# Kernel optimization log

Hardware: AMD Instinct MI355X
Metric: run time of the kernel (lower is better)

Reference implementation:

```python
import jax, jax.numpy as jnp
import numpy as np

B, H, W, CIN, COUT, KH, KW = 8, 256, 256, 64, 64, 3, 3

def setup_inputs() -> dict:
    key = jax.random.key(0)
    k1, k2 = jax.random.split(key)
    inputs = jax.random.normal(k1, (B, H, W, CIN), dtype=jnp.float32)
    kernel = jax.random.normal(k2, (CIN, COUT, KH, KW), dtype=jnp.float32)
    return {"inputs": inputs, "kernel": kernel}

def reference(inputs, kernel):
    # Stride-1 transposed convolution with 'full' output size:
    # out[b, p, q, co] = sum_{ci,i,j} inputs[b, i, j, ci] * kernel[ci, co, p-i, q-j]
    # which is a full (mathematical) convolution. lax performs cross-correlation,
    # so flip the kernel spatially and pad by (k-1) on each side.
    kh, kw = kernel.shape[2], kernel.shape[3]
    k_flipped = jnp.flip(kernel, axis=(2, 3))
    out = jax.lax.conv_general_dilated(
        inputs, k_flipped,
        window_strides=(1, 1),
        padding=[(kh - 1, kh - 1), (kw - 1, kw - 1)],
        dimension_numbers=("NHWC", "IOHW", "NHWC"))
    # out: [B, H+KH-1, W+KW-1, COUT]; original call() adds no bias.
    return out
```

## Files before the change

### kernel.cpp

```cpp
#include <hip/hip_runtime.h>
#include <hip/hip_bf16.h>


#define OH 258
#define OW 258

typedef __bf16 bf16x8 __attribute__((ext_vector_type(8)));
typedef float  f32x4  __attribute__((ext_vector_type(4)));

__global__ void prep_w_kernel(const float* __restrict__ k, __bf16* __restrict__ wsW) {
    int i = blockIdx.x * 256 + threadIdx.x;
    int c  = i & 31;
    int co = (i >> 5) & 63;
    int st = i >> 11;
    int s   = st & 1;
    int tap = st >> 1;
    int kh = tap / 3, kw = tap % 3;
    float v = k[(s * 32 + c) * 576 + co * 9 + kh * 3 + kw];
    wsW[i] = (__bf16)v;
}

__global__ __launch_bounds__(512, 4)
void tconv_kernel(const float* __restrict__ in, const __bf16* __restrict__ wsW,
                  float* __restrict__ out) {
    __shared__ __bf16 lds_in[612 * 64];

    const int tid = threadIdx.x;
    const int b  = blockIdx.z;
    const int p0 = blockIdx.y * 32;
    const int q0 = blockIdx.x * 16;

    #pragma unroll 1
    for (int it = tid; it < 612 * 8; it += 512) {
        int pix = it >> 3, c8 = it & 7;
        int r = pix / 18, c = pix - r * 18;
        int ip = p0 - 2 + r, iq = q0 - 2 + c;
        f32x4 v0 = {0.f,0.f,0.f,0.f}, v1 = {0.f,0.f,0.f,0.f};
        if ((unsigned)ip < 256u && (unsigned)iq < 256u) {
            const float* g = in + (((size_t)b * 256 + ip) * 256 + iq) * 64 + c8 * 8;
            v0 = *(const f32x4*)g;
            v1 = *(const f32x4*)(g + 4);
        }
        bf16x8 w;
        w[0]=(__bf16)v0[0]; w[1]=(__bf16)v0[1]; w[2]=(__bf16)v0[2]; w[3]=(__bf16)v0[3];
        w[4]=(__bf16)v1[0]; w[5]=(__bf16)v1[1]; w[6]=(__bf16)v1[2]; w[7]=(__bf16)v1[3];
        *(bf16x8*)&lds_in[pix * 64 + (c8 ^ (pix & 7)) * 8] = w;
    }
    __syncthreads();

    const int wv = tid >> 6, lane = tid & 63;
    const int ml = lane & 15, h = lane >> 4;
    const int woff = ml * 32 + h * 8;

    f32x4 acc[4][4] = {};

    #pragma unroll 1
    for (int tap = 0; tap < 9; ++tap) {
        const int kh = tap / 3, kw = tap - kh * 3;
        const __bf16* wt = wsW + tap * 4096;
        #pragma unroll
        for (int s = 0; s < 2; ++s) {
            bf16x8 bfr[4];
            #pragma unroll
            for (int nt = 0; nt < 4; ++nt)
                bfr[nt] = *(const bf16x8*)(wt + s * 2048 + nt * 512 + woff);
            const int j = s * 4 + h;
            #pragma unroll
            for (int mt = 0; mt < 4; ++mt) {
                int row = wv * 4 + mt + 2 - kh;
                int pix = row * 18 + (2 - kw) + ml;
                bf16x8 afr = *(const bf16x8*)&lds_in[pix * 64 + ((j ^ (pix & 7)) * 8)];
                #pragma unroll
                for (int nt = 0; nt < 4; ++nt)
                    acc[mt][nt] = __builtin_amdgcn_mfma_f32_16x16x32_bf16(
                        afr, bfr[nt], acc[mt][nt], 0, 0, 0);
            }
        }
    }

    #pragma unroll
    for (int mt = 0; mt < 4; ++mt) {
        int p = p0 + wv * 4 + mt;
        if (p < OH) {
            int qb = q0 + h * 4;
            #pragma unroll
            for (int nt = 0; nt < 4; ++nt) {
                float* op = out + (((size_t)b * OH + p) * OW + qb) * 64 + nt * 16 + ml;
                #pragma unroll
                for (int r = 0; r < 4; ++r)
                    if (qb + r < OW) op[(size_t)r * 64] = acc[mt][nt][r];
            }
        }
    }
}

extern "C" void kernel_launch(void* const* d_in, const int* in_sizes, int n_in,
                              void* d_out, int out_size, void* d_ws, size_t ws_size,
                              hipStream_t stream) {
    (void)in_sizes; (void)n_in; (void)out_size; (void)ws_size;
    const float* in   = (const float*)d_in[0];
    const float* kern = (const float*)d_in[1];
    float* out = (float*)d_out;
    __bf16* wsW = (__bf16*)d_ws;

    prep_w_kernel<<<144, 256, 0, stream>>>(kern, wsW);
    dim3 grid(17, 9, 8);
    tconv_kernel<<<grid, 512, 0, stream>>>(in, wsW, out);
}
```

Measured before the change: 277.7 us.

## Halve output tile height and batch global loads for more occupancy

Each block now covers 16 output rows instead of 32, which halves the LDS input tile (324 pixels instead of 612) and the per-wave accumulators. The grid grows to 17x17x8 and launch bounds ask for 6 blocks per CU. The staging loop is unrolled in groups of three so several global loads are in flight before the bf16 conversion and LDS stores. The cost is more halo recomputation per output row (18/16 instead of 34/32), more blocks, and fewer MFMAs per B-fragment load.

```diff
diff --git a/kernel.cpp b/kernel.cpp
--- a/kernel.cpp
+++ b/kernel.cpp
@@ -20,39 +20,57 @@
     wsW[i] = (__bf16)v;
 }
 
-__global__ __launch_bounds__(512, 4)
+__global__ __launch_bounds__(512, 6)
 void tconv_kernel(const float* __restrict__ in, const __bf16* __restrict__ wsW,
                   float* __restrict__ out) {
-    __shared__ __bf16 lds_in[612 * 64];
+    __shared__ __bf16 lds_in[324 * 64];
 
     const int tid = threadIdx.x;
     const int b  = blockIdx.z;
-    const int p0 = blockIdx.y * 32;
+    const int p0 = blockIdx.y * 16;
     const int q0 = blockIdx.x * 16;
 
     #pragma unroll 1
-    for (int it = tid; it < 612 * 8; it += 512) {
-        int pix = it >> 3, c8 = it & 7;
-        int r = pix / 18, c = pix - r * 18;
-        int ip = p0 - 2 + r, iq = q0 - 2 + c;
-        f32x4 v0 = {0.f,0.f,0.f,0.f}, v1 = {0.f,0.f,0.f,0.f};
-        if ((unsigned)ip < 256u && (unsigned)iq < 256u) {
-            const float* g = in + (((size_t)b * 256 + ip) * 256 + iq) * 64 + c8 * 8;
-            v0 = *(const f32x4*)g;
-            v1 = *(const f32x4*)(g + 4);
+    for (int kk = 0; kk < 6; kk += 3) {
+        f32x4 v0[3], v1[3];
+        int soff[3];
+        #pragma unroll
+        for (int u = 0; u < 3; ++u) {
+            const int k = kk + u;
+            const int it = tid + k * 512;
+            const bool act = (k < 5) || (tid < 32);
+            int pix = it >> 3, c8 = it & 7;
+            int r = pix / 18, c = pix - r * 18;
+            int ip = p0 - 2 + r, iq = q0 - 2 + c;
+            f32x4 z = {0.f, 0.f, 0.f, 0.f};
+            v0[u] = z; v1[u] = z;
+            if (act && (unsigned)ip < 256u && (unsigned)iq < 256u) {
+                const float* g = in + (((size_t)b * 256 + ip) * 256 + iq) * 64 + c8 * 8;
+                v0[u] = *(const f32x4*)g;
+                v1[u] = *(const f32x4*)(g + 4);
+            }
+            soff[u] = pix * 64 + ((c8 ^ (pix & 7)) * 8);
         }
-        bf16x8 w;
-        w[0]=(__bf16)v0[0]; w[1]=(__bf16)v0[1]; w[2]=(__bf16)v0[2]; w[3]=(__bf16)v0[3];
-        w[4]=(__bf16)v1[0]; w[5]=(__bf16)v1[1]; w[6]=(__bf16)v1[2]; w[7]=(__bf16)v1[3];
-        *(bf16x8*)&lds_in[pix * 64 + (c8 ^ (pix & 7)) * 8] = w;
+        #pragma unroll
+        for (int u = 0; u < 3; ++u) {
+            const int k = kk + u;
+            const bool act = (k < 5) || (tid < 32);
+            if (act) {
+                bf16x8 w;
+                w[0]=(__bf16)v0[u][0]; w[1]=(__bf16)v0[u][1]; w[2]=(__bf16)v0[u][2]; w[3]=(__bf16)v0[u][3];
+                w[4]=(__bf16)v1[u][0]; w[5]=(__bf16)v1[u][1]; w[6]=(__bf16)v1[u][2]; w[7]=(__bf16)v1[u][3];
+                *(bf16x8*)&lds_in[soff[u]] = w;
+            }
+        }
     }
     __syncthreads();
 
     const int wv = tid >> 6, lane = tid & 63;
     const int ml = lane & 15, h = lane >> 4;
     const int woff = ml * 32 + h * 8;
+    const int rbase = wv * 2;
 
-    f32x4 acc[4][4] = {};
+    f32x4 acc[2][4] = {};
 
     #pragma unroll 1
     for (int tap = 0; tap < 9; ++tap) {
@@ -66,8 +84,8 @@
                 bfr[nt] = *(const bf16x8*)(wt + s * 2048 + nt * 512 + woff);
             const int j = s * 4 + h;
             #pragma unroll
-            for (int mt = 0; mt < 4; ++mt) {
-                int row = wv * 4 + mt + 2 - kh;
+            for (int mt = 0; mt < 2; ++mt) {
+                int row = rbase + mt + 2 - kh;
                 int pix = row * 18 + (2 - kw) + ml;
                 bf16x8 afr = *(const bf16x8*)&lds_in[pix * 64 + ((j ^ (pix & 7)) * 8)];
                 #pragma unroll
@@ -79,8 +97,8 @@
     }
 
     #pragma unroll
-    for (int mt = 0; mt < 4; ++mt) {
-        int p = p0 + wv * 4 + mt;
+    for (int mt = 0; mt < 2; ++mt) {
+        int p = p0 + rbase + mt;
         if (p < OH) {
             int qb = q0 + h * 4;
             #pragma unroll
@@ -104,6 +122,6 @@
     __bf16* wsW = (__bf16*)d_ws;
 
     prep_w_kernel<<<144, 256, 0, stream>>>(kern, wsW);
-    dim3 grid(17, 9, 8);
+    dim3 grid(17, 17, 8);
     tconv_kernel<<<grid, 512, 0, stream>>>(in, wsW, out);
 }
```

Result: slower. 292.7 us (+5.4%).

## Drop LDS staging; load input fragments directly from global into registers

Applied to the files above, without the earlier changes.

Removes the shared-memory input tile and the block barrier. Each wave now loads its A fragments straight from global memory per kw and channel half, converts them to bf16 in registers, and reuses six rows across the three kh taps. Blocks shrink to 256 threads covering 16 output rows, which doubles the grid and changes the occupancy bound. The cost is redundant global and L2 traffic, since neighbouring waves and kw shifts reload overlapping input rows and the fp32-to-bf16 conversion is repeated for each reload.

```diff
diff --git a/kernel.cpp b/kernel.cpp
--- a/kernel.cpp
+++ b/kernel.cpp
@@ -20,67 +20,67 @@
     wsW[i] = (__bf16)v;
 }
 
-__global__ __launch_bounds__(512, 4)
+__global__ __launch_bounds__(256, 3)
 void tconv_kernel(const float* __restrict__ in, const __bf16* __restrict__ wsW,
                   float* __restrict__ out) {
-    __shared__ __bf16 lds_in[612 * 64];
-
     const int tid = threadIdx.x;
     const int b  = blockIdx.z;
-    const int p0 = blockIdx.y * 32;
+    const int p0 = blockIdx.y * 16;
     const int q0 = blockIdx.x * 16;
-
-    #pragma unroll 1
-    for (int it = tid; it < 612 * 8; it += 512) {
-        int pix = it >> 3, c8 = it & 7;
-        int r = pix / 18, c = pix - r * 18;
-        int ip = p0 - 2 + r, iq = q0 - 2 + c;
-        f32x4 v0 = {0.f,0.f,0.f,0.f}, v1 = {0.f,0.f,0.f,0.f};
-        if ((unsigned)ip < 256u && (unsigned)iq < 256u) {
-            const float* g = in + (((size_t)b * 256 + ip) * 256 + iq) * 64 + c8 * 8;
-            v0 = *(const f32x4*)g;
-            v1 = *(const f32x4*)(g + 4);
-        }
-        bf16x8 w;
-        w[0]=(__bf16)v0[0]; w[1]=(__bf16)v0[1]; w[2]=(__bf16)v0[2]; w[3]=(__bf16)v0[3];
-        w[4]=(__bf16)v1[0]; w[5]=(__bf16)v1[1]; w[6]=(__bf16)v1[2]; w[7]=(__bf16)v1[3];
-        *(bf16x8*)&lds_in[pix * 64 + (c8 ^ (pix & 7)) * 8] = w;
-    }
-    __syncthreads();
 
     const int wv = tid >> 6, lane = tid & 63;
     const int ml = lane & 15, h = lane >> 4;
     const int woff = ml * 32 + h * 8;
+    const int pw = p0 + wv * 4;
+
+    const float* inb = in + (size_t)b * (256 * 256 * 64);
 
     f32x4 acc[4][4] = {};
 
     #pragma unroll 1
-    for (int tap = 0; tap < 9; ++tap) {
-        const int kh = tap / 3, kw = tap - kh * 3;
-        const __bf16* wt = wsW + tap * 4096;
+    for (int kw = 0; kw < 3; ++kw) {
+        const int iqk = q0 + ml - kw;
+        const bool qok = (unsigned)iqk < 256u;
         #pragma unroll
         for (int s = 0; s < 2; ++s) {
-            bf16x8 bfr[4];
+            bf16x8 af[6];
             #pragma unroll
-            for (int nt = 0; nt < 4; ++nt)
-                bfr[nt] = *(const bf16x8*)(wt + s * 2048 + nt * 512 + woff);
-            const int j = s * 4 + h;
+            for (int d = 0; d < 6; ++d) {
+                const int ip = pw + d - 2;
+                f32x4 v0 = {0.f,0.f,0.f,0.f}, v1 = {0.f,0.f,0.f,0.f};
+                if (qok && (unsigned)ip < 256u) {
+                    const float* g = inb + ((size_t)(ip * 256 + iqk)) * 64
+                                         + s * 32 + h * 8;
+                    v0 = *(const f32x4*)g;
+                    v1 = *(const f32x4*)(g + 4);
+                }
+                bf16x8 w;
+                w[0]=(__bf16)v0[0]; w[1]=(__bf16)v0[1]; w[2]=(__bf16)v0[2]; w[3]=(__bf16)v0[3];
+                w[4]=(__bf16)v1[0]; w[5]=(__bf16)v1[1]; w[6]=(__bf16)v1[2]; w[7]=(__bf16)v1[3];
+                af[d] = w;
+            }
             #pragma unroll
-            for (int mt = 0; mt < 4; ++mt) {
-                int row = wv * 4 + mt + 2 - kh;
-                int pix = row * 18 + (2 - kw) + ml;
-                bf16x8 afr = *(const bf16x8*)&lds_in[pix * 64 + ((j ^ (pix & 7)) * 8)];
+            for (int kh = 0; kh < 3; ++kh) {
+                const __bf16* wt = wsW + (kh * 3 + kw) * 4096 + s * 2048 + woff;
+                bf16x8 bfr[4];
                 #pragma unroll
                 for (int nt = 0; nt < 4; ++nt)
-                    acc[mt][nt] = __builtin_amdgcn_mfma_f32_16x16x32_bf16(
-                        afr, bfr[nt], acc[mt][nt], 0, 0, 0);
+                    bfr[nt] = *(const bf16x8*)(wt + nt * 512);
+                #pragma unroll
+                for (int mt = 0; mt < 4; ++mt) {
+                    const bf16x8 a = af[mt - kh + 2];
+                    #pragma unroll
+                    for (int nt = 0; nt < 4; ++nt)
+                        acc[mt][nt] = __builtin_amdgcn_mfma_f32_16x16x32_bf16(
+                            a, bfr[nt], acc[mt][nt], 0, 0, 0);
+                }
             }
         }
     }
 
     #pragma unroll
     for (int mt = 0; mt < 4; ++mt) {
-        int p = p0 + wv * 4 + mt;
+        int p = pw + mt;
         if (p < OH) {
             int qb = q0 + h * 4;
             #pragma unroll
@@ -104,6 +104,6 @@
     __bf16* wsW = (__bf16*)d_ws;
 
     prep_w_kernel<<<144, 256, 0, stream>>>(kern, wsW);
-    dim3 grid(17, 9, 8);
-    tconv_kernel<<<grid, 512, 0, stream>>>(in, wsW, out);
+    dim3 grid(17, 17, 8);
+    tconv_kernel<<<grid, 256, 0, stream>>>(in, wsW, out);
 }
```

After: 304.9 us. +9.8%, slower.

## Stage weights in LDS, use 1024-thread blocks, vectorize output stores

Applied to the files above, without the earlier changes.

Doubles the block to 16 waves, each computing 2 output rows instead of 4, and copies all bf16 weights (about 72KB) into LDS next to the input tile. Swaps the MFMA operand order so each lane holds four consecutive channels of one pixel, which lets the epilogue write f32x4 vectors instead of scalar strided stores. This removes repeated global weight fetches and the scattered output writes, but LDS grows to roughly 150KB per block, so only one block fits per CU.

```diff
diff --git a/kernel.cpp b/kernel.cpp
--- a/kernel.cpp
+++ b/kernel.cpp
@@ -20,10 +20,11 @@
     wsW[i] = (__bf16)v;
 }
 
-__global__ __launch_bounds__(512, 4)
+__global__ __launch_bounds__(1024, 4)
 void tconv_kernel(const float* __restrict__ in, const __bf16* __restrict__ wsW,
                   float* __restrict__ out) {
     __shared__ __bf16 lds_in[612 * 64];
+    __shared__ __bf16 lds_w[36864];
 
     const int tid = threadIdx.x;
     const int b  = blockIdx.z;
@@ -31,33 +32,44 @@
     const int q0 = blockIdx.x * 16;
 
     #pragma unroll 1
-    for (int it = tid; it < 612 * 8; it += 512) {
+    for (int k = 0; k < 5; ++k) {
+        const int it = tid + k * 1024;
+        const bool act = (k < 4) || (tid < 800);
         int pix = it >> 3, c8 = it & 7;
         int r = pix / 18, c = pix - r * 18;
         int ip = p0 - 2 + r, iq = q0 - 2 + c;
         f32x4 v0 = {0.f,0.f,0.f,0.f}, v1 = {0.f,0.f,0.f,0.f};
-        if ((unsigned)ip < 256u && (unsigned)iq < 256u) {
+        if (act && (unsigned)ip < 256u && (unsigned)iq < 256u) {
             const float* g = in + (((size_t)b * 256 + ip) * 256 + iq) * 64 + c8 * 8;
             v0 = *(const f32x4*)g;
             v1 = *(const f32x4*)(g + 4);
         }
-        bf16x8 w;
-        w[0]=(__bf16)v0[0]; w[1]=(__bf16)v0[1]; w[2]=(__bf16)v0[2]; w[3]=(__bf16)v0[3];
-        w[4]=(__bf16)v1[0]; w[5]=(__bf16)v1[1]; w[6]=(__bf16)v1[2]; w[7]=(__bf16)v1[3];
-        *(bf16x8*)&lds_in[pix * 64 + (c8 ^ (pix & 7)) * 8] = w;
+        if (act) {
+            bf16x8 w;
+            w[0]=(__bf16)v0[0]; w[1]=(__bf16)v0[1]; w[2]=(__bf16)v0[2]; w[3]=(__bf16)v0[3];
+            w[4]=(__bf16)v1[0]; w[5]=(__bf16)v1[1]; w[6]=(__bf16)v1[2]; w[7]=(__bf16)v1[3];
+            *(bf16x8*)&lds_in[pix * 64 + (c8 ^ (pix & 7)) * 8] = w;
+        }
+    }
+    #pragma unroll
+    for (int k = 0; k < 5; ++k) {
+        const int g = tid + k * 1024;
+        if ((k < 4) || (tid < 512))
+            *(bf16x8*)&lds_w[(size_t)g * 8] = *(const bf16x8*)&wsW[(size_t)g * 8];
     }
     __syncthreads();
 
     const int wv = tid >> 6, lane = tid & 63;
     const int ml = lane & 15, h = lane >> 4;
     const int woff = ml * 32 + h * 8;
+    const int rbase = wv * 2;
 
-    f32x4 acc[4][4] = {};
+    f32x4 acc[2][4] = {};
 
     #pragma unroll 1
     for (int tap = 0; tap < 9; ++tap) {
         const int kh = tap / 3, kw = tap - kh * 3;
-        const __bf16* wt = wsW + tap * 4096;
+        const __bf16* wt = lds_w + tap * 4096;
         #pragma unroll
         for (int s = 0; s < 2; ++s) {
             bf16x8 bfr[4];
@@ -66,30 +78,27 @@
                 bfr[nt] = *(const bf16x8*)(wt + s * 2048 + nt * 512 + woff);
             const int j = s * 4 + h;
             #pragma unroll
-            for (int mt = 0; mt < 4; ++mt) {
-                int row = wv * 4 + mt + 2 - kh;
+            for (int mt = 0; mt < 2; ++mt) {
+                int row = rbase + mt + 2 - kh;
                 int pix = row * 18 + (2 - kw) + ml;
                 bf16x8 afr = *(const bf16x8*)&lds_in[pix * 64 + ((j ^ (pix & 7)) * 8)];
                 #pragma unroll
                 for (int nt = 0; nt < 4; ++nt)
                     acc[mt][nt] = __builtin_amdgcn_mfma_f32_16x16x32_bf16(
-                        afr, bfr[nt], acc[mt][nt], 0, 0, 0);
+                        bfr[nt], afr, acc[mt][nt], 0, 0, 0);
             }
         }
     }
 
+    const int q = q0 + ml;
     #pragma unroll
-    for (int mt = 0; mt < 4; ++mt) {
-        int p = p0 + wv * 4 + mt;
-        if (p < OH) {
-            int qb = q0 + h * 4;
+    for (int mt = 0; mt < 2; ++mt) {
+        int p = p0 + rbase + mt;
+        if (p < OH && q < OW) {
+            float* op = out + (((size_t)b * OH + p) * OW + q) * 64 + h * 4;
             #pragma unroll
-            for (int nt = 0; nt < 4; ++nt) {
-                float* op = out + (((size_t)b * OH + p) * OW + qb) * 64 + nt * 16 + ml;
-                #pragma unroll
-                for (int r = 0; r < 4; ++r)
-                    if (qb + r < OW) op[(size_t)r * 64] = acc[mt][nt][r];
-            }
+            for (int nt = 0; nt < 4; ++nt)
+                *(f32x4*)(op + nt * 16) = acc[mt][nt];
         }
     }
 }
@@ -105,5 +114,5 @@
 
     prep_w_kernel<<<144, 256, 0, stream>>>(kern, wsW);
     dim3 grid(17, 9, 8);
-    tconv_kernel<<<grid, 512, 0, stream>>>(in, wsW, out);
+    tconv_kernel<<<grid, 1024, 0, stream>>>(in, wsW, out);
 }
```

Measured after the change: 257.3 us. 7.3% less time.
